# Kernel tuning notes

Measured on AMD Instinct MI355X. Metric: run time of the kernel, lower is better.

Reference implementation:

```python
import jax, jax.numpy as jnp
import numpy as np


def setup_inputs() -> dict:
    key = jax.random.key(0)
    ks = jax.random.split(key, 5)
    T, B, C, H, K = 2048, 8, 1024, 16, 7
    s = 1.0 / np.sqrt(C)
    return {
        "x": jax.random.normal(ks[0], (T, B, C), dtype=jnp.float32),
        "w_weight": jax.random.normal(ks[1], (H * K, C), dtype=jnp.float32) * s,
        "glu_w": jax.random.normal(ks[2], (2 * H, C), dtype=jnp.float32) * s,
        "glu_b": jnp.zeros((2 * H,), dtype=jnp.float32),
        "out_w": jax.random.normal(ks[3], (C, C), dtype=jnp.float32) * s,
        "out_b": jnp.zeros((C,), dtype=jnp.float32),
        "padding_l": 6,
    }


def reference(x, w_weight, glu_w, glu_b, out_w, out_b, padding_l):
    # x: (T, B, C) in TBC format
    T, B, C = x.shape
    H = glu_w.shape[0] // 2
    K = w_weight.shape[0] // H
    R = C // H  # channels per head

    # GLU gate: C -> 2H, split last dim, a * sigmoid(b)  -> (T, B, H)
    g = (x @ glu_w.T + glu_b).reshape(T, B, H, 2)
    gate = g[..., 0] * jax.nn.sigmoid(g[..., 1])

    # per-position per-head kernel weights, softmax over K -> (T, B, H, K)
    w = jax.nn.softmax((x @ w_weight.T).reshape(T, B, H, K), axis=-1)

    # depthwise dynamic conv: out[t] = sum_k w[t,k] * x_pad[t + k]
    xh = x.reshape(T, B, H, R)
    xp = jnp.pad(xh, ((padding_l, K - 1 - padding_l), (0, 0), (0, 0), (0, 0)))
    conv = jnp.zeros_like(xh)
    for k in range(K):  # K is small & static; avoids (B,H,T,K,R) unfold blowup
        conv = conv + w[..., k:k + 1] * jax.lax.dynamic_slice_in_dim(xp, k, T, axis=0)

    # gate per head, merge heads, output projection
    out = (conv * gate[..., None]).reshape(T, B, C)
    return out @ out_w.T + out_b
```

## Files before the change

kernel.cpp:

```cpp
#include <hip/hip_runtime.h>
#include <hip/hip_bf16.h>
#include <stdint.h>

#define T_DIM 2048
#define B_DIM 8
#define C_DIM 1024
#define H_DIM 16
#define K_DIM 7
#define M_DIM (T_DIM * B_DIM)
#define NLOG 144

typedef __attribute__((ext_vector_type(8))) short short8;
typedef __attribute__((ext_vector_type(4))) float floatx4;

__device__ __forceinline__ float bf2f(uint32_t u) {
    union { uint32_t i; float f; } v; v.i = u << 16; return v.f;
}
__device__ __forceinline__ ushort f2bf(float f) {
    __hip_bfloat16 h = __float2bfloat16(f);
    return *(ushort*)&h;
}

#define S_X  ((size_t)M_DIM * C_DIM)
#define S_W  ((size_t)112 * C_DIM)
#define S_G  ((size_t)32 * C_DIM)
#define S_O  ((size_t)C_DIM * C_DIM)
#define S_TOT (S_X + S_W + S_G + S_O)

__global__ __launch_bounds__(256) void cvt_kernel(
    const float* __restrict__ x, const float* __restrict__ w_weight,
    const float* __restrict__ glu_w, const float* __restrict__ out_w,
    ushort* __restrict__ xb, ushort* __restrict__ wb, ushort* __restrict__ Wb)
{
    size_t gid = ((size_t)blockIdx.x * 256 + threadIdx.x) * 4;
    const float* src; ushort* dst; size_t off;
    if (gid < S_X)                   { src = x;        dst = xb;        off = gid; }
    else if (gid < S_X + S_W)        { src = w_weight; dst = wb;        off = gid - S_X; }
    else if (gid < S_X + S_W + S_G)  { src = glu_w;    dst = wb + S_W;  off = gid - S_X - S_W; }
    else                             { src = out_w;    dst = Wb;        off = gid - S_X - S_W - S_G; }
    float4 v = *(const float4*)(src + off);
    ushort4 o; o.x = f2bf(v.x); o.y = f2bf(v.y); o.z = f2bf(v.z); o.w = f2bf(v.w);
    *(ushort4*)(dst + off) = o;
}

__global__ __launch_bounds__(256) void logits_kernel(
    const ushort* __restrict__ xb,
    const ushort* __restrict__ wb,
    float* __restrict__ logits)
{
    const int wave = threadIdx.x >> 6;
    const int lane = threadIdx.x & 63;
    const int m0 = (blockIdx.x * 4 + wave) * 16;
    const int fr = lane & 15;
    const int q  = lane >> 4;

    floatx4 acc[9];
#pragma unroll
    for (int j = 0; j < 9; ++j) acc[j] = (floatx4){0.f, 0.f, 0.f, 0.f};

    const ushort* arow = xb + (size_t)(m0 + fr) * C_DIM + q * 8;
    const ushort* brow = wb + (size_t)fr * C_DIM + q * 8;

    for (int k0 = 0; k0 < C_DIM; k0 += 32) {
        short8 a = *(const short8*)(arow + k0);
#pragma unroll
        for (int j = 0; j < 9; ++j) {
            short8 b = *(const short8*)(brow + (size_t)j * 16 * C_DIM + k0);
            acc[j] = __builtin_amdgcn_mfma_f32_16x16x32_bf16(a, b, acc[j], 0, 0, 0);
        }
    }

#pragma unroll
    for (int j = 0; j < 9; ++j) {
        int n = j * 16 + fr;
#pragma unroll
        for (int r = 0; r < 4; ++r) {
            int m = m0 + q * 4 + r;
            logits[(size_t)m * NLOG + n] = acc[j][r];
        }
    }
}

__global__ __launch_bounds__(64) void conv_kernel(
    const ushort* __restrict__ xb,
    const float* __restrict__ logits,
    const float* __restrict__ glu_b,
    const int* __restrict__ padding_l_,
    ushort* __restrict__ y)
{
    const int tb = blockIdx.x;
    const int t = tb / B_DIM, b = tb % B_DIM;
    const int lane = threadIdx.x;
    const int pad = *padding_l_;

    __shared__ float wsm[H_DIM][K_DIM];
    __shared__ float gsm[H_DIM];

    if (lane < H_DIM) {
        const float* lg = logits + (size_t)tb * NLOG;
        float l0[K_DIM];
        float mx = -1e30f;
#pragma unroll
        for (int k = 0; k < K_DIM; ++k) { l0[k] = lg[lane * K_DIM + k]; mx = fmaxf(mx, l0[k]); }
        float s = 0.f;
#pragma unroll
        for (int k = 0; k < K_DIM; ++k) { l0[k] = __expf(l0[k] - mx); s += l0[k]; }
        float inv = 1.f / s;
#pragma unroll
        for (int k = 0; k < K_DIM; ++k) wsm[lane][k] = l0[k] * inv;
        float ga = lg[112 + 2 * lane]     + glu_b[2 * lane];
        float gb = lg[112 + 2 * lane + 1] + glu_b[2 * lane + 1];
        gsm[lane] = ga * (1.f / (1.f + __expf(-gb)));
    }
    __syncthreads();

    const int c0 = lane * 16;
    const int h = lane >> 2;
    float accv[16];
#pragma unroll
    for (int i = 0; i < 16; ++i) accv[i] = 0.f;

    for (int k = 0; k < K_DIM; ++k) {
        int ts = t + k - pad;
        if (ts < 0 || ts >= T_DIM) continue;
        float wk = wsm[h][k];
        const uint4* xp = (const uint4*)(xb + ((size_t)ts * B_DIM + b) * C_DIM + c0);
        uint4 v0 = xp[0], v1 = xp[1];
        uint32_t u[8] = {v0.x, v0.y, v0.z, v0.w, v1.x, v1.y, v1.z, v1.w};
#pragma unroll
        for (int i = 0; i < 8; ++i) {
            accv[2 * i]     += wk * bf2f(u[i] & 0xffffu);
            accv[2 * i + 1] += wk * bf2f(u[i] >> 16);
        }
    }

    float g = gsm[h];
    uint32_t o[8];
#pragma unroll
    for (int i = 0; i < 8; ++i) {
        o[i] = (uint32_t)f2bf(accv[2 * i] * g) | ((uint32_t)f2bf(accv[2 * i + 1] * g) << 16);
    }
    uint4* yr = (uint4*)(y + (size_t)tb * C_DIM + c0);
    yr[0] = (uint4){o[0], o[1], o[2], o[3]};
    yr[1] = (uint4){o[4], o[5], o[6], o[7]};
}

__global__ __launch_bounds__(256) void out_gemm(
    const ushort* __restrict__ y,
    const ushort* __restrict__ Wb,
    const float* __restrict__ bias,
    float* __restrict__ out)
{
    __shared__ __align__(16) ushort As[128 * 64];
    __shared__ __align__(16) ushort Bs[128 * 64];

    const int bn = blockIdx.x & 7;
    const int bm = blockIdx.x >> 3;
    const int m0 = bm * 128, n0 = bn * 128;
    const int tid = threadIdx.x;
    const int lane = tid & 63, wave = tid >> 6;
    const int wm = (wave >> 1) * 64, wn = (wave & 1) * 64;
    const int fr = lane & 15, q = lane >> 4;

    floatx4 acc[4][4];
#pragma unroll
    for (int i = 0; i < 4; ++i)
#pragma unroll
        for (int j = 0; j < 4; ++j) acc[i][j] = (floatx4){0.f, 0.f, 0.f, 0.f};

    for (int k0 = 0; k0 < C_DIM; k0 += 64) {
        __syncthreads();
#pragma unroll
        for (int j = 0; j < 4; ++j) {
            int idx = j * 256 + tid;
            int r = idx >> 3, ch = idx & 7;
            const ushort* ga = y + (size_t)(m0 + r) * C_DIM + k0 + ch * 8;
            __builtin_amdgcn_global_load_lds(
                (const __attribute__((address_space(1))) void*)ga,
                (__attribute__((address_space(3))) void*)(As + idx * 8), 16, 0, 0);
            const ushort* gb = Wb + (size_t)(n0 + r) * C_DIM + k0 + ch * 8;
            __builtin_amdgcn_global_load_lds(
                (const __attribute__((address_space(1))) void*)gb,
                (__attribute__((address_space(3))) void*)(Bs + idx * 8), 16, 0, 0);
        }
        __syncthreads();

#pragma unroll
        for (int s = 0; s < 64; s += 32) {
            short8 a[4], b[4];
#pragma unroll
            for (int i = 0; i < 4; ++i)
                a[i] = *(const short8*)(As + (wm + i * 16 + fr) * 64 + s + q * 8);
#pragma unroll
            for (int j = 0; j < 4; ++j)
                b[j] = *(const short8*)(Bs + (wn + j * 16 + fr) * 64 + s + q * 8);
#pragma unroll
            for (int i = 0; i < 4; ++i)
#pragma unroll
                for (int j = 0; j < 4; ++j)
                    acc[i][j] = __builtin_amdgcn_mfma_f32_16x16x32_bf16(a[i], b[j], acc[i][j], 0, 0, 0);
        }
    }

#pragma unroll
    for (int j = 0; j < 4; ++j) {
        int n = n0 + wn + j * 16 + fr;
        float bv = bias[n];
#pragma unroll
        for (int i = 0; i < 4; ++i) {
#pragma unroll
            for (int r = 0; r < 4; ++r) {
                int m = m0 + wm + i * 16 + q * 4 + r;
                out[(size_t)m * C_DIM + n] = acc[i][j][r] + bv;
            }
        }
    }
}

extern "C" void kernel_launch(void* const* d_in, const int* in_sizes, int n_in,
                              void* d_out, int out_size, void* d_ws, size_t ws_size,
                              hipStream_t stream) {
    const float* x        = (const float*)d_in[0];
    const float* w_weight = (const float*)d_in[1];
    const float* glu_w    = (const float*)d_in[2];
    const float* glu_b    = (const float*)d_in[3];
    const float* out_w    = (const float*)d_in[4];
    const float* out_b    = (const float*)d_in[5];
    const int* padding_l  = (const int*)d_in[6];
    float* out = (float*)d_out;

    char* ws = (char*)d_ws;
    ushort* xb    = (ushort*)ws;
    ushort* y     = xb + S_X;
    ushort* wb    = y + S_X;
    ushort* Wb    = wb + S_W + S_G;
    float* logits = (float*)(Wb + S_O);

    cvt_kernel<<<(S_TOT / 4 + 255) / 256, 256, 0, stream>>>(x, w_weight, glu_w, out_w, xb, wb, Wb);
    logits_kernel<<<M_DIM / 64, 256, 0, stream>>>(xb, wb, logits);
    conv_kernel<<<M_DIM, 64, 0, stream>>>(xb, logits, glu_b, padding_l, y);
    out_gemm<<<(M_DIM / 128) * (C_DIM / 128), 256, 0, stream>>>(y, Wb, out_b, out);
}
```

Baseline: 261.6 us.

## Fuse logits GEMM with softmax/conv, drop x bf16 conversion, swizzle out_gemm LDS

Stops converting the large activation tensor x to bf16 and instead converts it on the fly inside a new fused kernel. That kernel computes the gate/weight logits with MFMA (split-K across waves, reduced through shared memory), applies softmax and GLU, and runs the dynamic conv directly from fp32 x. This removes the xb and logits round-trips through global memory and two kernel launches. The output GEMM also gets an XOR swizzle on LDS to avoid bank conflicts and an M-major block order for better reuse of the weight tile; the conv now reads fp32 x, which doubles its read bytes.

```diff
diff --git a/kernel.cpp b/kernel.cpp
--- a/kernel.cpp
+++ b/kernel.cpp
@@ -13,136 +13,131 @@
 typedef __attribute__((ext_vector_type(8))) short short8;
 typedef __attribute__((ext_vector_type(4))) float floatx4;
 
-__device__ __forceinline__ float bf2f(uint32_t u) {
-    union { uint32_t i; float f; } v; v.i = u << 16; return v.f;
-}
 __device__ __forceinline__ ushort f2bf(float f) {
     __hip_bfloat16 h = __float2bfloat16(f);
     return *(ushort*)&h;
 }
 
-#define S_X  ((size_t)M_DIM * C_DIM)
 #define S_W  ((size_t)112 * C_DIM)
 #define S_G  ((size_t)32 * C_DIM)
 #define S_O  ((size_t)C_DIM * C_DIM)
-#define S_TOT (S_X + S_W + S_G + S_O)
-
-__global__ __launch_bounds__(256) void cvt_kernel(
-    const float* __restrict__ x, const float* __restrict__ w_weight,
-    const float* __restrict__ glu_w, const float* __restrict__ out_w,
-    ushort* __restrict__ xb, ushort* __restrict__ wb, ushort* __restrict__ Wb)
+#define S_WG (S_W + S_G)
+#define S_CVT (S_WG + S_O)
+
+__global__ __launch_bounds__(256) void cvt_w_kernel(
+    const float* __restrict__ w_weight, const float* __restrict__ glu_w,
+    const float* __restrict__ out_w,
+    ushort* __restrict__ wb, ushort* __restrict__ Wb)
 {
     size_t gid = ((size_t)blockIdx.x * 256 + threadIdx.x) * 4;
     const float* src; ushort* dst; size_t off;
-    if (gid < S_X)                   { src = x;        dst = xb;        off = gid; }
-    else if (gid < S_X + S_W)        { src = w_weight; dst = wb;        off = gid - S_X; }
-    else if (gid < S_X + S_W + S_G)  { src = glu_w;    dst = wb + S_W;  off = gid - S_X - S_W; }
-    else                             { src = out_w;    dst = Wb;        off = gid - S_X - S_W - S_G; }
+    if (gid < S_W)            { src = w_weight; dst = wb;       off = gid; }
+    else if (gid < S_WG)      { src = glu_w;    dst = wb + S_W; off = gid - S_W; }
+    else                      { src = out_w;    dst = Wb;       off = gid - S_WG; }
     float4 v = *(const float4*)(src + off);
     ushort4 o; o.x = f2bf(v.x); o.y = f2bf(v.y); o.z = f2bf(v.z); o.w = f2bf(v.w);
     *(ushort4*)(dst + off) = o;
 }
 
-__global__ __launch_bounds__(256) void logits_kernel(
-    const ushort* __restrict__ xb,
+__global__ __launch_bounds__(256) void fused_logits_conv(
+    const float* __restrict__ x,
     const ushort* __restrict__ wb,
-    float* __restrict__ logits)
-{
-    const int wave = threadIdx.x >> 6;
-    const int lane = threadIdx.x & 63;
-    const int m0 = (blockIdx.x * 4 + wave) * 16;
-    const int fr = lane & 15;
-    const int q  = lane >> 4;
-
-    floatx4 acc[9];
-#pragma unroll
-    for (int j = 0; j < 9; ++j) acc[j] = (floatx4){0.f, 0.f, 0.f, 0.f};
-
-    const ushort* arow = xb + (size_t)(m0 + fr) * C_DIM + q * 8;
-    const ushort* brow = wb + (size_t)fr * C_DIM + q * 8;
-
-    for (int k0 = 0; k0 < C_DIM; k0 += 32) {
-        short8 a = *(const short8*)(arow + k0);
-#pragma unroll
-        for (int j = 0; j < 9; ++j) {
-            short8 b = *(const short8*)(brow + (size_t)j * 16 * C_DIM + k0);
-            acc[j] = __builtin_amdgcn_mfma_f32_16x16x32_bf16(a, b, acc[j], 0, 0, 0);
-        }
-    }
-
-#pragma unroll
-    for (int j = 0; j < 9; ++j) {
-        int n = j * 16 + fr;
-#pragma unroll
-        for (int r = 0; r < 4; ++r) {
-            int m = m0 + q * 4 + r;
-            logits[(size_t)m * NLOG + n] = acc[j][r];
-        }
-    }
-}
-
-__global__ __launch_bounds__(64) void conv_kernel(
-    const ushort* __restrict__ xb,
-    const float* __restrict__ logits,
     const float* __restrict__ glu_b,
     const int* __restrict__ padding_l_,
     ushort* __restrict__ y)
 {
-    const int tb = blockIdx.x;
-    const int t = tb / B_DIM, b = tb % B_DIM;
-    const int lane = threadIdx.x;
+    __shared__ float part[4][16][NLOG];
+    __shared__ float wk[16][H_DIM][K_DIM];
+    __shared__ float gg[16][H_DIM];
+
+    const int tid = threadIdx.x;
+    const int wave = tid >> 6, lane = tid & 63;
+    const int fr = lane & 15, q = lane >> 4;
+    const int m0 = blockIdx.x * 16;
+
+    floatx4 acc[9];
+#pragma unroll
+    for (int j = 0; j < 9; ++j) acc[j] = (floatx4){0.f, 0.f, 0.f, 0.f};
+
+    const float* arow  = x  + (size_t)(m0 + fr) * C_DIM + wave * 256 + q * 8;
+    const ushort* brow = wb + (size_t)fr * C_DIM        + wave * 256 + q * 8;
+
+#pragma unroll
+    for (int it = 0; it < 8; ++it) {
+        float4 v0 = *(const float4*)(arow + it * 32);
+        float4 v1 = *(const float4*)(arow + it * 32 + 4);
+        short8 a;
+        a[0] = (short)f2bf(v0.x); a[1] = (short)f2bf(v0.y);
+        a[2] = (short)f2bf(v0.z); a[3] = (short)f2bf(v0.w);
+        a[4] = (short)f2bf(v1.x); a[5] = (short)f2bf(v1.y);
+        a[6] = (short)f2bf(v1.z); a[7] = (short)f2bf(v1.w);
+#pragma unroll
+        for (int j = 0; j < 9; ++j) {
+            short8 b = *(const short8*)(brow + (size_t)j * 16 * C_DIM + it * 32);
+            acc[j] = __builtin_amdgcn_mfma_f32_16x16x32_bf16(a, b, acc[j], 0, 0, 0);
+        }
+    }
+#pragma unroll
+    for (int j = 0; j < 9; ++j)
+#pragma unroll
+        for (int r = 0; r < 4; ++r)
+            part[wave][q * 4 + r][j * 16 + fr] = acc[j][r];
+    __syncthreads();
+
+    {
+        const int row = tid >> 4, h = tid & 15;
+        float l[K_DIM];
+        float mx = -1e30f;
+#pragma unroll
+        for (int k = 0; k < K_DIM; ++k) {
+            float s = part[0][row][h * K_DIM + k] + part[1][row][h * K_DIM + k]
+                    + part[2][row][h * K_DIM + k] + part[3][row][h * K_DIM + k];
+            l[k] = s; mx = fmaxf(mx, s);
+        }
+        float s = 0.f;
+#pragma unroll
+        for (int k = 0; k < K_DIM; ++k) { l[k] = __expf(l[k] - mx); s += l[k]; }
+        float inv = 1.f / s;
+#pragma unroll
+        for (int k = 0; k < K_DIM; ++k) wk[row][h][k] = l[k] * inv;
+        float ga = part[0][row][112 + 2 * h] + part[1][row][112 + 2 * h]
+                 + part[2][row][112 + 2 * h] + part[3][row][112 + 2 * h] + glu_b[2 * h];
+        float gb = part[0][row][113 + 2 * h] + part[1][row][113 + 2 * h]
+                 + part[2][row][113 + 2 * h] + part[3][row][113 + 2 * h] + glu_b[2 * h + 1];
+        gg[row][h] = ga * (1.f / (1.f + __expf(-gb)));
+    }
+    __syncthreads();
+
     const int pad = *padding_l_;
-
-    __shared__ float wsm[H_DIM][K_DIM];
-    __shared__ float gsm[H_DIM];
-
-    if (lane < H_DIM) {
-        const float* lg = logits + (size_t)tb * NLOG;
-        float l0[K_DIM];
-        float mx = -1e30f;
-#pragma unroll
-        for (int k = 0; k < K_DIM; ++k) { l0[k] = lg[lane * K_DIM + k]; mx = fmaxf(mx, l0[k]); }
-        float s = 0.f;
-#pragma unroll
-        for (int k = 0; k < K_DIM; ++k) { l0[k] = __expf(l0[k] - mx); s += l0[k]; }
-        float inv = 1.f / s;
-#pragma unroll
-        for (int k = 0; k < K_DIM; ++k) wsm[lane][k] = l0[k] * inv;
-        float ga = lg[112 + 2 * lane]     + glu_b[2 * lane];
-        float gb = lg[112 + 2 * lane + 1] + glu_b[2 * lane + 1];
-        gsm[lane] = ga * (1.f / (1.f + __expf(-gb)));
-    }
-    __syncthreads();
-
     const int c0 = lane * 16;
     const int h = lane >> 2;
-    float accv[16];
-#pragma unroll
-    for (int i = 0; i < 16; ++i) accv[i] = 0.f;
-
-    for (int k = 0; k < K_DIM; ++k) {
-        int ts = t + k - pad;
-        if (ts < 0 || ts >= T_DIM) continue;
-        float wk = wsm[h][k];
-        const uint4* xp = (const uint4*)(xb + ((size_t)ts * B_DIM + b) * C_DIM + c0);
-        uint4 v0 = xp[0], v1 = xp[1];
-        uint32_t u[8] = {v0.x, v0.y, v0.z, v0.w, v1.x, v1.y, v1.z, v1.w};
-#pragma unroll
-        for (int i = 0; i < 8; ++i) {
-            accv[2 * i]     += wk * bf2f(u[i] & 0xffffu);
-            accv[2 * i + 1] += wk * bf2f(u[i] >> 16);
-        }
-    }
-
-    float g = gsm[h];
-    uint32_t o[8];
-#pragma unroll
-    for (int i = 0; i < 8; ++i) {
-        o[i] = (uint32_t)f2bf(accv[2 * i] * g) | ((uint32_t)f2bf(accv[2 * i + 1] * g) << 16);
-    }
-    uint4* yr = (uint4*)(y + (size_t)tb * C_DIM + c0);
-    yr[0] = (uint4){o[0], o[1], o[2], o[3]};
-    yr[1] = (uint4){o[4], o[5], o[6], o[7]};
+    for (int rr = wave; rr < 16; rr += 4) {
+        const int m = m0 + rr;
+        const int t = m >> 3;
+        float av[16];
+#pragma unroll
+        for (int i = 0; i < 16; ++i) av[i] = 0.f;
+#pragma unroll
+        for (int k = 0; k < K_DIM; ++k) {
+            int ts = t + k - pad;
+            if (ts < 0 || ts >= T_DIM) continue;
+            float wv = wk[rr][h][k];
+            const float4* xp = (const float4*)(x + ((size_t)m + 8 * (k - pad)) * C_DIM + c0);
+            float4 u0 = xp[0], u1 = xp[1], u2 = xp[2], u3 = xp[3];
+            av[0]  += wv * u0.x; av[1]  += wv * u0.y; av[2]  += wv * u0.z; av[3]  += wv * u0.w;
+            av[4]  += wv * u1.x; av[5]  += wv * u1.y; av[6]  += wv * u1.z; av[7]  += wv * u1.w;
+            av[8]  += wv * u2.x; av[9]  += wv * u2.y; av[10] += wv * u2.z; av[11] += wv * u2.w;
+            av[12] += wv * u3.x; av[13] += wv * u3.y; av[14] += wv * u3.z; av[15] += wv * u3.w;
+        }
+        float g = gg[rr][h];
+        uint32_t o[8];
+#pragma unroll
+        for (int i = 0; i < 8; ++i)
+            o[i] = (uint32_t)f2bf(av[2 * i] * g) | ((uint32_t)f2bf(av[2 * i + 1] * g) << 16);
+        uint4* yr = (uint4*)(y + (size_t)m * C_DIM + c0);
+        yr[0] = (uint4){o[0], o[1], o[2], o[3]};
+        yr[1] = (uint4){o[4], o[5], o[6], o[7]};
+    }
 }
 
 __global__ __launch_bounds__(256) void out_gemm(
@@ -154,8 +149,8 @@
     __shared__ __align__(16) ushort As[128 * 64];
     __shared__ __align__(16) ushort Bs[128 * 64];
 
-    const int bn = blockIdx.x & 7;
-    const int bm = blockIdx.x >> 3;
+    const int bm = blockIdx.x & 127;
+    const int bn = blockIdx.x >> 7;
     const int m0 = bm * 128, n0 = bn * 128;
     const int tid = threadIdx.x;
     const int lane = tid & 63, wave = tid >> 6;
@@ -173,7 +168,8 @@
 #pragma unroll
         for (int j = 0; j < 4; ++j) {
             int idx = j * 256 + tid;
-            int r = idx >> 3, ch = idx & 7;
+            int r = idx >> 3, cl = idx & 7;
+            int ch = cl ^ (r & 7);
             const ushort* ga = y + (size_t)(m0 + r) * C_DIM + k0 + ch * 8;
             __builtin_amdgcn_global_load_lds(
                 (const __attribute__((address_space(1))) void*)ga,
@@ -187,13 +183,18 @@
 
 #pragma unroll
         for (int s = 0; s < 64; s += 32) {
+            const int cbase = (s >> 3) + q;
             short8 a[4], b[4];
 #pragma unroll
-            for (int i = 0; i < 4; ++i)
-                a[i] = *(const short8*)(As + (wm + i * 16 + fr) * 64 + s + q * 8);
-#pragma unroll
-            for (int j = 0; j < 4; ++j)
-                b[j] = *(const short8*)(Bs + (wn + j * 16 + fr) * 64 + s + q * 8);
+            for (int i = 0; i < 4; ++i) {
+                int r = wm + i * 16 + fr;
+                a[i] = *(const short8*)(As + r * 64 + ((cbase ^ (r & 7)) * 8));
+            }
+#pragma unroll
+            for (int j = 0; j < 4; ++j) {
+                int r = wn + j * 16 + fr;
+                b[j] = *(const short8*)(Bs + r * 64 + ((cbase ^ (r & 7)) * 8));
+            }
 #pragma unroll
             for (int i = 0; i < 4; ++i)
 #pragma unroll
@@ -230,14 +231,11 @@
     float* out = (float*)d_out;
 
     char* ws = (char*)d_ws;
-    ushort* xb    = (ushort*)ws;
-    ushort* y     = xb + S_X;
-    ushort* wb    = y + S_X;
-    ushort* Wb    = wb + S_W + S_G;
-    float* logits = (float*)(Wb + S_O);
-
-    cvt_kernel<<<(S_TOT / 4 + 255) / 256, 256, 0, stream>>>(x, w_weight, glu_w, out_w, xb, wb, Wb);
-    logits_kernel<<<M_DIM / 64, 256, 0, stream>>>(xb, wb, logits);
-    conv_kernel<<<M_DIM, 64, 0, stream>>>(xb, logits, glu_b, padding_l, y);
+    ushort* y  = (ushort*)ws;
+    ushort* wb = y + (size_t)M_DIM * C_DIM;
+    ushort* Wb = wb + S_WG;
+
+    cvt_w_kernel<<<S_CVT / 4 / 256, 256, 0, stream>>>(w_weight, glu_w, out_w, wb, Wb);
+    fused_logits_conv<<<M_DIM / 16, 256, 0, stream>>>(x, wb, glu_b, padding_l, y);
     out_gemm<<<(M_DIM / 128) * (C_DIM / 128), 256, 0, stream>>>(y, Wb, out_b, out);
 }
```

New measurement: 244.6 us. -6.5%, faster.
